# Kernel optimization log

Hardware: AMD Instinct MI355X
Metric: run time of the kernel (lower is better)

## Reference

```python
import jax, jax.numpy as jnp
import numpy as np


def _silu(x):
    return x * jax.nn.sigmoid(x)


def setup_inputs() -> dict:
    key = jax.random.key(0)
    ks = jax.random.split(key, 8)
    B, S, H, E, I, IS = 2, 1024, 2048, 64, 512, 1024
    s = 0.02  # weight init scale to keep activations in a sane range
    return {
        "hidden_states": jax.random.normal(ks[0], (B, S, H), jnp.float32),
        "gate_weight": jax.random.normal(ks[1], (E, H), jnp.float32) * s,   # router [E,H]
        "w_gate": jax.random.normal(ks[2], (E, H, I), jnp.float32) * s,
        "w_up": jax.random.normal(ks[3], (E, H, I), jnp.float32) * s,
        "w_down": jax.random.normal(ks[4], (E, I, H), jnp.float32) * s,
        "sw_gate": jax.random.normal(ks[5], (H, IS), jnp.float32) * s,
        "sw_up": jax.random.normal(ks[6], (H, IS), jnp.float32) * s,
        "sw_down": jax.random.normal(ks[7], (IS, H), jnp.float32) * s,
        "top_k": 6,
    }


def reference(hidden_states, gate_weight, w_gate, w_up, w_down,
              sw_gate, sw_up, sw_down, top_k):
    orig_shape = hidden_states.shape
    H = orig_shape[-1]
    x = hidden_states.reshape(-1, H)          # [T,H]
    T = x.shape[0]
    E = gate_weight.shape[0]

    # fp32 router (need_fp32_gate)
    logits = x.astype(jnp.float32) @ gate_weight.astype(jnp.float32).T   # [T,E]
    # sigmoid_routing_function: sigmoid -> normalize -> topk -> renormalize
    p = jax.nn.sigmoid(logits)
    p = p / jnp.sum(p, axis=-1, keepdims=True)
    topk_w, topk_idx = jax.lax.top_k(p, top_k)                           # [T,k]
    topk_w = topk_w / jnp.sum(topk_w, axis=-1, keepdims=True)            # renormalize

    # dense combine weights [T,E]: zero for unselected experts
    cw = jnp.zeros((T, E), x.dtype).at[jnp.arange(T)[:, None], topk_idx].set(
        topk_w.astype(x.dtype))

    # grouped SwiGLU expert FFN, combine weighted outputs; scan over experts
    # keeps peak memory at one [T,I] intermediate per step.
    def step(acc, ew):
        wg, wu, wd, c = ew                                               # c: [T]
        y = (_silu(x @ wg) * (x @ wu)) @ wd                              # [T,H]
        return acc + c[:, None] * y, None

    routed, _ = jax.lax.scan(step, jnp.zeros_like(x),
                             (w_gate, w_up, w_down, cw.T))

    # shared experts FFN over all tokens (returned separately, not reduced)
    shared_out = (_silu(x @ sw_gate) * (x @ sw_up)) @ sw_down            # [T,H]

    return shared_out, routed.reshape(orig_shape)
```

## Files before the change

### kernel.cpp

```cpp
#include <hip/hip_runtime.h>
#include <hip/hip_bf16.h>
#include <stdint.h>


#define H_DIM 2048
#define E_NUM 64
#define I_DIM 512
#define IS_DIM 1024
#define CAPR 288
#define TOPK_MAX 8
#define BK 64
#define LDP 68

typedef float f32x4 __attribute__((ext_vector_type(4)));
typedef __bf16 bf16x8 __attribute__((ext_vector_type(8)));

__device__ __forceinline__ uint16_t f2bf(float f) {
  union { float f; uint32_t u; } v;
  v.f = f;
  uint32_t r = (v.u + 0x7FFFu + ((v.u >> 16) & 1u)) >> 16;
  return (uint16_t)r;
}
__device__ __forceinline__ uint32_t pack2(float a, float b) {
  return (uint32_t)f2bf(a) | ((uint32_t)f2bf(b) << 16);
}
__device__ __forceinline__ float bf2f(uint16_t b) {
  union { uint32_t u; float f; } v;
  v.u = (uint32_t)b << 16;
  return v.f;
}

#define BAR()                                              \
  do {                                                     \
    asm volatile("s_waitcnt lgkmcnt(0)" ::: "memory");     \
    __builtin_amdgcn_s_barrier();                          \
    asm volatile("" ::: "memory");                         \
  } while (0)

__global__ __launch_bounds__(256) void router_kernel(
    const float* __restrict__ x, const float* __restrict__ gw,
    const int* __restrict__ topk_ptr, int* __restrict__ cnt,
    int* __restrict__ bucket, float* __restrict__ bw,
    uint16_t* __restrict__ xbK, const int T) {
  const int t = blockIdx.x;
  const int tid = threadIdx.x;
  __shared__ float xs[H_DIM];
  __shared__ float logits[E_NUM];
#pragma unroll
  for (int i = 0; i < 2; ++i) {
    int idx = tid + i * 256;
    *(float4*)(&xs[idx * 4]) = *(const float4*)(x + (size_t)t * H_DIM + idx * 4);
  }
  __syncthreads();
  {
    const float* p = &xs[tid * 8];
    uint4 o;
    o.x = pack2(p[0], p[1]);
    o.y = pack2(p[2], p[3]);
    o.z = pack2(p[4], p[5]);
    o.w = pack2(p[6], p[7]);
    *(uint4*)(xbK + (size_t)(tid >> 2) * T * 32 + (size_t)t * 32 +
              (tid & 3) * 8) = o;
  }
  const int lane = tid & 63, wid = tid >> 6;
  float xr[32];
#pragma unroll
  for (int it = 0; it < 32; ++it) xr[it] = xs[lane + 64 * it];
  for (int eo = 0; eo < 16; ++eo) {
    int e = wid + eo * 4;
    const float* g = gw + (size_t)e * H_DIM;
    float acc = 0.f;
#pragma unroll
    for (int it = 0; it < 32; ++it) acc += xr[it] * g[lane + 64 * it];
#pragma unroll
    for (int off = 32; off; off >>= 1) acc += __shfl_xor(acc, off);
    if (lane == 0) logits[e] = acc;
  }
  __syncthreads();
  if (wid == 0) {
    int k = topk_ptr[0];
    if (k > TOPK_MAX) k = TOPK_MAX;
    float v = 1.f / (1.f + expf(-logits[lane]));
    float s = 0.f, myw = 0.f;
    int mye = 0;
    for (int j = 0; j < k; ++j) {
      float m = v;
      int mi = lane;
#pragma unroll
      for (int off = 32; off; off >>= 1) {
        float ov = __shfl_xor(m, off);
        int oi = __shfl_xor(mi, off);
        if (ov > m || (ov == m && oi < mi)) { m = ov; mi = oi; }
      }
      if (lane == j) { myw = m; mye = mi; }
      if (lane == mi) v = -1e30f;
      s += m;
    }
    if (lane < k) {
      float w = myw / s;
      int pos = atomicAdd(&cnt[mye], 1);
      if (pos < CAPR) {
        bucket[mye * CAPR + pos] = t * 8 + lane;
        bw[mye * CAPR + pos] = w;
      }
    }
  }
}

__global__ __launch_bounds__(256) void gather_xe(
    const uint16_t* __restrict__ xbK, const int* __restrict__ cnt,
    const int* __restrict__ bucket, uint16_t* __restrict__ xe, const int T) {
  const int e = blockIdx.x;
  const int kgrp = blockIdx.y & 15, sgrp = blockIdx.y >> 4;
  const int tid = threadIdx.x;
  const int slot = sgrp * 64 + (tid & 63);
  const int kblk = kgrp * 4 + (tid >> 6);
  const int n_e = min(cnt[e], CAPR);
  if (slot >= n_e) return;
  const int t = bucket[e * CAPR + slot] >> 3;
  const uint4* src = (const uint4*)(xbK + (size_t)kblk * T * 32 + (size_t)t * 32);
  uint4* dst = (uint4*)(xe + (size_t)e * (64 * CAPR * 32) +
                        (size_t)kblk * (CAPR * 32) + (size_t)slot * 32);
#pragma unroll
  for (int j = 0; j < 4; ++j) dst[j] = src[j];
}

template <int BM, bool GATHER>
__global__ __launch_bounds__(256) void ffn_in(
    const uint16_t* __restrict__ A0, const float* __restrict__ Wg,
    const float* __restrict__ Wu, uint16_t* __restrict__ actO,
    const int* __restrict__ cnt, const int K, const int ldb, const int SLOTS) {
  constexpr int BN = 32;
  constexpr int MF = BM / 64;
  constexpr int NF = 2;

  int e = 0, nt, mt0, mtE, n_e;
  const float *Bg, *Bu;
  const uint16_t* AE;
  uint16_t* outE;
  if constexpr (GATHER) {
    e = blockIdx.x;
    nt = blockIdx.y;
    n_e = min(cnt[e], CAPR);
    mt0 = 0;
    mtE = (n_e + BM - 1) / BM;
    const size_t wo = (size_t)e * K * ldb;
    Bg = Wg + wo;
    Bu = Wu + wo;
    AE = A0 + (size_t)e * (64 * CAPR * 32);
    outE = actO + (size_t)e * ((I_DIM / 32) * CAPR * 32);
  } else {
    nt = blockIdx.x;
    mt0 = blockIdx.y;
    mtE = mt0 + 1;
    n_e = 1 << 30;
    Bg = Wg;
    Bu = Wu;
    AE = A0;
    outE = actO;
  }
  if (mt0 * BM >= n_e) return;

  __shared__ uint16_t Bgs[2][BN][LDP];
  __shared__ uint16_t Bus[2][BN][LDP];

  const int tid = threadIdx.x;
  const int cg4 = (tid & 7) * 4, kp = tid >> 3;
  const float* bgp = Bg + (size_t)(2 * kp) * ldb + nt * BN + cg4;
  const float* bup = Bu + (size_t)(2 * kp) * ldb + nt * BN + cg4;

  const int lane = tid & 63, wid = tid >> 6;
  const int fr = lane & 15, kg = lane >> 4;
  const int wrow = wid * (BM / 4);
  const size_t ldA = (size_t)SLOTS * 32;

  float4 g0, g1, u0, u1;
  const int NS = K / BK;

  for (int mt = mt0; mt < mtE; ++mt) {
    const uint16_t* ab[MF];
#pragma unroll
    for (int mf = 0; mf < MF; ++mf)
      ab[mf] = AE + (size_t)(mt * BM + wrow + mf * 16 + fr) * 32 + kg * 8;

    f32x4 accg[MF][NF] = {};
    f32x4 accu[MF][NF] = {};

    g0 = *(const float4*)bgp;
    g1 = *(const float4*)(bgp + ldb);
    u0 = *(const float4*)bup;
    u1 = *(const float4*)(bup + ldb);
    {
      const int k2 = 2 * kp;
      *(uint32_t*)(&Bgs[0][cg4 + 0][k2]) = pack2(g0.x, g1.x);
      *(uint32_t*)(&Bgs[0][cg4 + 1][k2]) = pack2(g0.y, g1.y);
      *(uint32_t*)(&Bgs[0][cg4 + 2][k2]) = pack2(g0.z, g1.z);
      *(uint32_t*)(&Bgs[0][cg4 + 3][k2]) = pack2(g0.w, g1.w);
      *(uint32_t*)(&Bus[0][cg4 + 0][k2]) = pack2(u0.x, u1.x);
      *(uint32_t*)(&Bus[0][cg4 + 1][k2]) = pack2(u0.y, u1.y);
      *(uint32_t*)(&Bus[0][cg4 + 2][k2]) = pack2(u0.z, u1.z);
      *(uint32_t*)(&Bus[0][cg4 + 3][k2]) = pack2(u0.w, u1.w);
    }
    if (NS > 1) {
      const float* g = bgp + (size_t)BK * ldb;
      g0 = *(const float4*)g;
      g1 = *(const float4*)(g + ldb);
      const float* u = bup + (size_t)BK * ldb;
      u0 = *(const float4*)u;
      u1 = *(const float4*)(u + ldb);
    }
    BAR();

    int b = 0;
    for (int s = 0; s < NS; ++s) {
      uint4 a[MF][2];
#pragma unroll
      for (int mf = 0; mf < MF; ++mf)
#pragma unroll
        for (int sl = 0; sl < 2; ++sl)
          a[mf][sl] = *(const uint4*)(ab[mf] + (size_t)(2 * s + sl) * ldA);
      if (s + 1 < NS) {
        const int k2 = 2 * kp;
        *(uint32_t*)(&Bgs[b ^ 1][cg4 + 0][k2]) = pack2(g0.x, g1.x);
        *(uint32_t*)(&Bgs[b ^ 1][cg4 + 1][k2]) = pack2(g0.y, g1.y);
        *(uint32_t*)(&Bgs[b ^ 1][cg4 + 2][k2]) = pack2(g0.z, g1.z);
        *(uint32_t*)(&Bgs[b ^ 1][cg4 + 3][k2]) = pack2(g0.w, g1.w);
        *(uint32_t*)(&Bus[b ^ 1][cg4 + 0][k2]) = pack2(u0.x, u1.x);
        *(uint32_t*)(&Bus[b ^ 1][cg4 + 1][k2]) = pack2(u0.y, u1.y);
        *(uint32_t*)(&Bus[b ^ 1][cg4 + 2][k2]) = pack2(u0.z, u1.z);
        *(uint32_t*)(&Bus[b ^ 1][cg4 + 3][k2]) = pack2(u0.w, u1.w);
      }
      if (s + 2 < NS) {
        const float* g = bgp + (size_t)((s + 2) * BK) * ldb;
        g0 = *(const float4*)g;
        g1 = *(const float4*)(g + ldb);
        const float* u = bup + (size_t)((s + 2) * BK) * ldb;
        u0 = *(const float4*)u;
        u1 = *(const float4*)(u + ldb);
      }
#pragma unroll
      for (int sl = 0; sl < 2; ++sl)
#pragma unroll
        for (int nf = 0; nf < NF; ++nf) {
          const bf16x8 bg = __builtin_bit_cast(
              bf16x8, *(const uint4*)(&Bgs[b][nf * 16 + fr][kg * 8 + sl * 32]));
          const bf16x8 bu = __builtin_bit_cast(
              bf16x8, *(const uint4*)(&Bus[b][nf * 16 + fr][kg * 8 + sl * 32]));
#pragma unroll
          for (int mf = 0; mf < MF; ++mf) {
            const bf16x8 af = __builtin_bit_cast(bf16x8, a[mf][sl]);
            accg[mf][nf] = __builtin_amdgcn_mfma_f32_16x16x32_bf16(
                af, bg, accg[mf][nf], 0, 0, 0);
            accu[mf][nf] = __builtin_amdgcn_mfma_f32_16x16x32_bf16(
                af, bu, accu[mf][nf], 0, 0, 0);
          }
        }
      BAR();
      b ^= 1;
    }

#pragma unroll
    for (int mf = 0; mf < MF; ++mf)
#pragma unroll
      for (int rr = 0; rr < 4; ++rr) {
        const int slot = mt * BM + wrow + mf * 16 + kg * 4 + rr;
        if (slot < n_e) {
          uint16_t* op = outE + (size_t)nt * ldA + (size_t)slot * 32 + fr;
#pragma unroll
          for (int nf = 0; nf < NF; ++nf) {
            const float g = accg[mf][nf][rr], u = accu[mf][nf][rr];
            op[nf * 16] = f2bf(g / (1.f + expf(-g)) * u);
          }
        }
      }
  }
}

template <int BM, bool GATHER>
__global__ __launch_bounds__(256) void ffn_down(
    const uint16_t* __restrict__ A0, const float* __restrict__ Wd,
    void* __restrict__ outp, const int* __restrict__ cnt,
    const int* __restrict__ bucket, const float* __restrict__ bw,
    const int K, const int SLOTS) {
  constexpr int BN = 64;
  constexpr int MF = BM / 64;
  constexpr int NF = 4;

  int e = 0, nt, mt0, mtE, n_e;
  const float* Bd;
  const uint16_t* AE;
  if constexpr (GATHER) {
    e = blockIdx.x;
    nt = blockIdx.y;
    n_e = min(cnt[e], CAPR);
    mt0 = 0;
    mtE = (n_e + BM - 1) / BM;
    AE = A0 + (size_t)e * ((I_DIM / 32) * CAPR * 32);
    Bd = Wd + (size_t)e * K * H_DIM;
  } else {
    nt = blockIdx.x;
    mt0 = blockIdx.y;
    mtE = mt0 + 1;
    n_e = 1 << 30;
    AE = A0;
    Bd = Wd;
  }
  if (mt0 * BM >= n_e) return;

  __shared__ uint16_t Bs[2][BN][LDP];

  const int tid = threadIdx.x;
  const int cg4 = (tid & 15) * 4, kp = tid >> 4;
  const float* bdp = Bd + (size_t)(2 * kp) * H_DIM + nt * BN + cg4;

  const int lane = tid & 63, wid = tid >> 6;
  const int fr = lane & 15, kg = lane >> 4;
  const int wrow = wid * (BM / 4);
  const size_t ldA = (size_t)SLOTS * 32;

  float4 d0[2], d1[2];
  const int NS = K / BK;

  for (int mt = mt0; mt < mtE; ++mt) {
    const uint16_t* ab[MF];
#pragma unroll
    for (int mf = 0; mf < MF; ++mf)
      ab[mf] = AE + (size_t)(mt * BM + wrow + mf * 16 + fr) * 32 + kg * 8;

    f32x4 acc[MF][NF] = {};

#pragma unroll
    for (int pp = 0; pp < 2; ++pp) {
      const float* d = bdp + (size_t)(2 * pp * 16) * H_DIM;
      d0[pp] = *(const float4*)d;
      d1[pp] = *(const float4*)(d + H_DIM);
    }
#pragma unroll
    for (int pp = 0; pp < 2; ++pp) {
      const int k2 = 2 * (kp + pp * 16);
      *(uint32_t*)(&Bs[0][cg4 + 0][k2]) = pack2(d0[pp].x, d1[pp].x);
      *(uint32_t*)(&Bs[0][cg4 + 1][k2]) = pack2(d0[pp].y, d1[pp].y);
      *(uint32_t*)(&Bs[0][cg4 + 2][k2]) = pack2(d0[pp].z, d1[pp].z);
      *(uint32_t*)(&Bs[0][cg4 + 3][k2]) = pack2(d0[pp].w, d1[pp].w);
    }
    if (NS > 1) {
#pragma unroll
      for (int pp = 0; pp < 2; ++pp) {
        const float* d = bdp + (size_t)(BK + 2 * pp * 16) * H_DIM;
        d0[pp] = *(const float4*)d;
        d1[pp] = *(const float4*)(d + H_DIM);
      }
    }
    BAR();

    int b = 0;
    for (int s = 0; s < NS; ++s) {
      uint4 a[MF][2];
#pragma unroll
      for (int mf = 0; mf < MF; ++mf)
#pragma unroll
        for (int sl = 0; sl < 2; ++sl)
          a[mf][sl] = *(const uint4*)(ab[mf] + (size_t)(2 * s + sl) * ldA);
      if (s + 1 < NS) {
#pragma unroll
        for (int pp = 0; pp < 2; ++pp) {
          const int k2 = 2 * (kp + pp * 16);
          *(uint32_t*)(&Bs[b ^ 1][cg4 + 0][k2]) = pack2(d0[pp].x, d1[pp].x);
          *(uint32_t*)(&Bs[b ^ 1][cg4 + 1][k2]) = pack2(d0[pp].y, d1[pp].y);
          *(uint32_t*)(&Bs[b ^ 1][cg4 + 2][k2]) = pack2(d0[pp].z, d1[pp].z);
          *(uint32_t*)(&Bs[b ^ 1][cg4 + 3][k2]) = pack2(d0[pp].w, d1[pp].w);
        }
      }
      if (s + 2 < NS) {
#pragma unroll
        for (int pp = 0; pp < 2; ++pp) {
          const float* d = bdp + (size_t)((s + 2) * BK + 2 * pp * 16) * H_DIM;
          d0[pp] = *(const float4*)d;
          d1[pp] = *(const float4*)(d + H_DIM);
        }
      }
#pragma unroll
      for (int sl = 0; sl < 2; ++sl)
#pragma unroll
        for (int nf = 0; nf < NF; ++nf) {
          const bf16x8 bf_ = __builtin_bit_cast(
              bf16x8, *(const uint4*)(&Bs[b][nf * 16 + fr][kg * 8 + sl * 32]));
#pragma unroll
          for (int mf = 0; mf < MF; ++mf) {
            const bf16x8 af = __builtin_bit_cast(bf16x8, a[mf][sl]);
            acc[mf][nf] = __builtin_amdgcn_mfma_f32_16x16x32_bf16(
                af, bf_, acc[mf][nf], 0, 0, 0);
          }
        }
      BAR();
      b ^= 1;
    }

    const int col0 = nt * BN + fr;
#pragma unroll
    for (int mf = 0; mf < MF; ++mf)
#pragma unroll
      for (int rr = 0; rr < 4; ++rr) {
        const int slot = mt * BM + wrow + mf * 16 + kg * 4 + rr;
        if constexpr (GATHER) {
          if (slot < n_e) {
            const int bv = bucket[e * CAPR + slot];
            const float w = bw[e * CAPR + slot];
            uint16_t* yb = (uint16_t*)outp + (size_t)bv * H_DIM + col0;
#pragma unroll
            for (int nf = 0; nf < NF; ++nf)
              yb[nf * 16] = f2bf(w * acc[mf][nf][rr]);
          }
        } else {
          float* op = (float*)outp + (size_t)slot * H_DIM + col0;
#pragma unroll
          for (int nf = 0; nf < NF; ++nf) op[nf * 16] = acc[mf][nf][rr];
        }
      }
  }
}

__global__ __launch_bounds__(256) void combine_kernel(
    const uint16_t* __restrict__ ybuf, const int* __restrict__ topk_ptr,
    float* __restrict__ routed) {
  const int t = blockIdx.x;
  const int tid = threadIdx.x;
  int k = topk_ptr[0];
  if (k > TOPK_MAX) k = TOPK_MAX;
  float acc[8] = {};
  const uint16_t* base = ybuf + (size_t)t * 8 * H_DIM + tid * 8;
  for (int j = 0; j < k; ++j) {
    uint4 v = *(const uint4*)(base + (size_t)j * H_DIM);
    const uint16_t* h = (const uint16_t*)&v;
#pragma unroll
    for (int i = 0; i < 8; ++i) acc[i] += bf2f(h[i]);
  }
  float* op = routed + (size_t)t * H_DIM + tid * 8;
  *(float4*)op = make_float4(acc[0], acc[1], acc[2], acc[3]);
  *(float4*)(op + 4) = make_float4(acc[4], acc[5], acc[6], acc[7]);
}

extern "C" void kernel_launch(void* const* d_in, const int* in_sizes, int n_in,
                              void* d_out, int out_size, void* d_ws, size_t ws_size,
                              hipStream_t stream) {
  const float* x = (const float*)d_in[0];
  const float* gw = (const float*)d_in[1];
  const float* w_gate = (const float*)d_in[2];
  const float* w_up = (const float*)d_in[3];
  const float* w_down = (const float*)d_in[4];
  const float* sw_gate = (const float*)d_in[5];
  const float* sw_up = (const float*)d_in[6];
  const float* sw_down = (const float*)d_in[7];
  const int* topk = (const int*)d_in[8];
  const int T = in_sizes[0] / H_DIM;

  float* shared_out = (float*)d_out;
  float* routed = shared_out + (size_t)T * H_DIM;

  char* ws = (char*)d_ws;
  size_t off = 0;
  auto take = [&](size_t b) {
    char* p = ws + off;
    off += (b + 255) & ~(size_t)255;
    return p;
  };
  uint16_t* xbK = (uint16_t*)take((size_t)T * H_DIM * 2);
  int* cnt = (int*)take(E_NUM * 4);
  int* bucket = (int*)take((size_t)E_NUM * CAPR * 4);
  float* bw = (float*)take((size_t)E_NUM * CAPR * 4);
  uint16_t* xe = (uint16_t*)take((size_t)E_NUM * 64 * CAPR * 32 * 2 + 65536);
  uint16_t* act = (uint16_t*)take((size_t)E_NUM * 16 * CAPR * 32 * 2 + 65536);
  uint16_t* s_act = (uint16_t*)take((size_t)(IS_DIM / 32) * T * 32 * 2);
  uint16_t* ybuf = (uint16_t*)take((size_t)T * 8 * H_DIM * 2);

  hipMemsetAsync(cnt, 0, E_NUM * 4, stream);

  router_kernel<<<T, 256, 0, stream>>>(x, gw, topk, cnt, bucket, bw, xbK, T);
  gather_xe<<<dim3(E_NUM, 16 * ((CAPR + 63) / 64)), 256, 0, stream>>>(
      xbK, cnt, bucket, xe, T);

  ffn_in<256, true><<<dim3(E_NUM, I_DIM / 32), 256, 0, stream>>>(
      xe, w_gate, w_up, act, cnt, H_DIM, I_DIM, CAPR);
  ffn_down<256, true><<<dim3(E_NUM, H_DIM / 64), 256, 0, stream>>>(
      act, w_down, (void*)ybuf, cnt, bucket, bw, I_DIM, CAPR);
  combine_kernel<<<T, 256, 0, stream>>>(ybuf, topk, routed);
  ffn_in<128, false><<<dim3(IS_DIM / 32, T / 128), 256, 0, stream>>>(
      xbK, sw_gate, sw_up, s_act, nullptr, H_DIM, IS_DIM, T);
  ffn_down<128, false><<<dim3(H_DIM / 64, T / 128), 256, 0, stream>>>(
      s_act, sw_down, (void*)shared_out, nullptr, nullptr, nullptr, IS_DIM, T);
}
```

Before: 440.5 us.

## Merge routed and shared expert GEMMs into combined grid launches

Folds the routed-expert and shared-expert up-projection kernels into one launch, and the two down-projection kernels into another. A block-index split picks which body each block runs. This lets the shared-expert blocks fill the CUs left idle by the many early-exiting or unevenly loaded routed-expert blocks, and removes two launch boundaries. The cost is that both bodies share one shared-memory and register allocation, and the index decoding relies on hardcoded widths (64 experts, 32 tiles).

```diff
diff --git a/kernel.cpp b/kernel.cpp
--- a/kernel.cpp
+++ b/kernel.cpp
@@ -126,11 +126,12 @@
 }
 
 template <int BM, bool GATHER>
-__global__ __launch_bounds__(256) void ffn_in(
+__device__ __forceinline__ void ffn_in_body(
+    uint16_t (*Bgs)[32][LDP], uint16_t (*Bus)[32][LDP],
     const uint16_t* __restrict__ A0, const float* __restrict__ Wg,
     const float* __restrict__ Wu, uint16_t* __restrict__ actO,
-    const int* __restrict__ cnt, const int K, const int ldb, const int SLOTS) {
-  constexpr int BN = 32;
+    const int* __restrict__ cnt, const int K, const int ldb, const int SLOTS,
+    const int bid) {
   constexpr int MF = BM / 64;
   constexpr int NF = 2;
 
@@ -139,8 +140,8 @@
   const uint16_t* AE;
   uint16_t* outE;
   if constexpr (GATHER) {
-    e = blockIdx.x;
-    nt = blockIdx.y;
+    e = bid & 63;
+    nt = bid >> 6;
     n_e = min(cnt[e], CAPR);
     mt0 = 0;
     mtE = (n_e + BM - 1) / BM;
@@ -150,8 +151,8 @@
     AE = A0 + (size_t)e * (64 * CAPR * 32);
     outE = actO + (size_t)e * ((I_DIM / 32) * CAPR * 32);
   } else {
-    nt = blockIdx.x;
-    mt0 = blockIdx.y;
+    nt = bid & 31;
+    mt0 = bid >> 5;
     mtE = mt0 + 1;
     n_e = 1 << 30;
     Bg = Wg;
@@ -161,13 +162,10 @@
   }
   if (mt0 * BM >= n_e) return;
 
-  __shared__ uint16_t Bgs[2][BN][LDP];
-  __shared__ uint16_t Bus[2][BN][LDP];
-
   const int tid = threadIdx.x;
   const int cg4 = (tid & 7) * 4, kp = tid >> 3;
-  const float* bgp = Bg + (size_t)(2 * kp) * ldb + nt * BN + cg4;
-  const float* bup = Bu + (size_t)(2 * kp) * ldb + nt * BN + cg4;
+  const float* bgp = Bg + (size_t)(2 * kp) * ldb + nt * 32 + cg4;
+  const float* bup = Bu + (size_t)(2 * kp) * ldb + nt * 32 + cg4;
 
   const int lane = tid & 63, wid = tid >> 6;
   const int fr = lane & 15, kg = lane >> 4;
@@ -276,13 +274,30 @@
   }
 }
 
+__global__ __launch_bounds__(256) void fused_in(
+    const uint16_t* __restrict__ xe, const float* __restrict__ Wg,
+    const float* __restrict__ Wu, uint16_t* __restrict__ act,
+    const int* __restrict__ cnt,
+    const uint16_t* __restrict__ xbK, const float* __restrict__ sWg,
+    const float* __restrict__ sWu, uint16_t* __restrict__ s_actK, const int T) {
+  __shared__ uint16_t Bgs[2][32][LDP];
+  __shared__ uint16_t Bus[2][32][LDP];
+  const int bx = blockIdx.x;
+  if (bx < E_NUM * (I_DIM / 32)) {
+    ffn_in_body<256, true>(Bgs, Bus, xe, Wg, Wu, act, cnt, H_DIM, I_DIM, CAPR,
+                           bx);
+  } else {
+    ffn_in_body<128, false>(Bgs, Bus, xbK, sWg, sWu, s_actK, nullptr, H_DIM,
+                            IS_DIM, T, bx - E_NUM * (I_DIM / 32));
+  }
+}
+
 template <int BM, bool GATHER>
-__global__ __launch_bounds__(256) void ffn_down(
-    const uint16_t* __restrict__ A0, const float* __restrict__ Wd,
-    void* __restrict__ outp, const int* __restrict__ cnt,
-    const int* __restrict__ bucket, const float* __restrict__ bw,
-    const int K, const int SLOTS) {
-  constexpr int BN = 64;
+__device__ __forceinline__ void ffn_down_body(
+    uint16_t (*Bs)[64][LDP], const uint16_t* __restrict__ A0,
+    const float* __restrict__ Wd, void* __restrict__ outp,
+    const int* __restrict__ cnt, const int* __restrict__ bucket,
+    const float* __restrict__ bw, const int K, const int SLOTS, const int bid) {
   constexpr int MF = BM / 64;
   constexpr int NF = 4;
 
@@ -290,16 +305,16 @@
   const float* Bd;
   const uint16_t* AE;
   if constexpr (GATHER) {
-    e = blockIdx.x;
-    nt = blockIdx.y;
+    e = bid & 63;
+    nt = bid >> 6;
     n_e = min(cnt[e], CAPR);
     mt0 = 0;
     mtE = (n_e + BM - 1) / BM;
     AE = A0 + (size_t)e * ((I_DIM / 32) * CAPR * 32);
     Bd = Wd + (size_t)e * K * H_DIM;
   } else {
-    nt = blockIdx.x;
-    mt0 = blockIdx.y;
+    nt = bid & 31;
+    mt0 = bid >> 5;
     mtE = mt0 + 1;
     n_e = 1 << 30;
     AE = A0;
@@ -307,11 +322,9 @@
   }
   if (mt0 * BM >= n_e) return;
 
-  __shared__ uint16_t Bs[2][BN][LDP];
-
   const int tid = threadIdx.x;
   const int cg4 = (tid & 15) * 4, kp = tid >> 4;
-  const float* bdp = Bd + (size_t)(2 * kp) * H_DIM + nt * BN + cg4;
+  const float* bdp = Bd + (size_t)(2 * kp) * H_DIM + nt * 64 + cg4;
 
   const int lane = tid & 63, wid = tid >> 6;
   const int fr = lane & 15, kg = lane >> 4;
@@ -396,7 +409,7 @@
       b ^= 1;
     }
 
-    const int col0 = nt * BN + fr;
+    const int col0 = nt * 64 + fr;
 #pragma unroll
     for (int mf = 0; mf < MF; ++mf)
 #pragma unroll
@@ -417,6 +430,24 @@
           for (int nf = 0; nf < NF; ++nf) op[nf * 16] = acc[mf][nf][rr];
         }
       }
+  }
+}
+
+__global__ __launch_bounds__(256) void fused_down(
+    const uint16_t* __restrict__ act, const float* __restrict__ Wd,
+    uint16_t* __restrict__ ybuf, const int* __restrict__ cnt,
+    const int* __restrict__ bucket, const float* __restrict__ bw,
+    const uint16_t* __restrict__ s_actK, const float* __restrict__ sWd,
+    float* __restrict__ shared_out, const int T) {
+  __shared__ uint16_t Bs[2][64][LDP];
+  const int bx = blockIdx.x;
+  if (bx < E_NUM * (H_DIM / 64)) {
+    ffn_down_body<256, true>(Bs, act, Wd, (void*)ybuf, cnt, bucket, bw, I_DIM,
+                             CAPR, bx);
+  } else {
+    ffn_down_body<128, false>(Bs, s_actK, sWd, (void*)shared_out, nullptr,
+                              nullptr, nullptr, IS_DIM, T,
+                              bx - E_NUM * (H_DIM / 64));
   }
 }
 
@@ -470,7 +501,7 @@
   float* bw = (float*)take((size_t)E_NUM * CAPR * 4);
   uint16_t* xe = (uint16_t*)take((size_t)E_NUM * 64 * CAPR * 32 * 2 + 65536);
   uint16_t* act = (uint16_t*)take((size_t)E_NUM * 16 * CAPR * 32 * 2 + 65536);
-  uint16_t* s_act = (uint16_t*)take((size_t)(IS_DIM / 32) * T * 32 * 2);
+  uint16_t* s_actK = (uint16_t*)take((size_t)(IS_DIM / 32) * T * 32 * 2);
   uint16_t* ybuf = (uint16_t*)take((size_t)T * 8 * H_DIM * 2);
 
   hipMemsetAsync(cnt, 0, E_NUM * 4, stream);
@@ -479,13 +510,9 @@
   gather_xe<<<dim3(E_NUM, 16 * ((CAPR + 63) / 64)), 256, 0, stream>>>(
       xbK, cnt, bucket, xe, T);
 
-  ffn_in<256, true><<<dim3(E_NUM, I_DIM / 32), 256, 0, stream>>>(
-      xe, w_gate, w_up, act, cnt, H_DIM, I_DIM, CAPR);
-  ffn_down<256, true><<<dim3(E_NUM, H_DIM / 64), 256, 0, stream>>>(
-      act, w_down, (void*)ybuf, cnt, bucket, bw, I_DIM, CAPR);
+  fused_in<<<E_NUM * (I_DIM / 32) + (IS_DIM / 32) * (T / 128), 256, 0, stream>>>(
+      xe, w_gate, w_up, act, cnt, xbK, sw_gate, sw_up, s_actK, T);
+  fused_down<<<E_NUM * (H_DIM / 64) + (H_DIM / 64) * (T / 128), 256, 0, stream>>>(
+      act, w_down, ybuf, cnt, bucket, bw, s_actK, sw_down, shared_out, T);
   combine_kernel<<<T, 256, 0, stream>>>(ybuf, topk, routed);
-  ffn_in<128, false><<<dim3(IS_DIM / 32, T / 128), 256, 0, stream>>>(
-      xbK, sw_gate, sw_up, s_act, nullptr, H_DIM, IS_DIM, T);
-  ffn_down<128, false><<<dim3(H_DIM / 64, T / 128), 256, 0, stream>>>(
-      s_act, sw_down, (void*)shared_out, nullptr, nullptr, nullptr, IS_DIM, T);
-}
+}
```

After: 511.9 us. 1.16x slower.
